# Performance work log

Measured on AMD Instinct MI355X. Metric: run time of the kernel, lower is better.

Reference implementation:

```python
import jax, jax.numpy as jnp
import numpy as np

TEMP = 0.05
EPS_SOFTMAX = 1e-6
EPS_LOG = 1e-6


def setup_inputs() -> dict:
    key = jax.random.key(0)
    k1, k2, k3, k4, k5 = jax.random.split(key, 5)
    B, F, N, C = 256, 128, 200000, 1000
    inputs = jax.random.normal(k1, (B, F), dtype=jnp.float32)
    inputs_s = jax.random.normal(k2, (B, F), dtype=jnp.float32)
    features = jax.random.normal(k3, (N, F), dtype=jnp.float32)
    # memory banks are kept L2-normalized (see MB.backward renorm)
    features = features / jnp.linalg.norm(features, axis=1, keepdims=True)
    labels = jax.random.randint(k4, (N,), 0, C, dtype=jnp.int64)
    indexes = jax.random.randint(k5, (B,), 0, N, dtype=jnp.int64)
    return {"inputs": inputs, "inputs_s": inputs_s, "features": features,
            "labels": labels, "indexes": indexes, "k": 10, "num_classes": C}


def reference(inputs, inputs_s, features, labels, indexes, k, num_classes):
    B = inputs.shape[0]
    N = features.shape[0]
    # features is a buffer (no grad in torch); MB backward also treats it as constant
    feats = jax.lax.stop_gradient(features)

    # MB.forward: inputs @ features.T, then /temp  -> [B, N]
    inputs_out = (inputs @ feats.T) / TEMP

    # local similarity [B, B]
    local = inputs @ inputs_s.T
    # topk neighbors in the bank, gather + per-sample bmm, sum over k -> [B, 1]
    _, nb_idx = jax.lax.top_k(inputs_out, k)          # [B, k]
    nb_ftr = feats[nb_idx]                             # [B, k, F]
    _local = jnp.einsum('bf,bkf->b', inputs, nb_ftr)[:, None]  # [B, 1]
    # (local + _local) masked to diagonal, then /temp
    local = (local + _local) * jnp.eye(B, dtype=local.dtype)
    local = local / TEMP

    targets = labels[indexes]                          # [B]

    # label-bucketed segment reductions -> sim [C, B]
    sim = jax.ops.segment_sum(inputs_out.T, labels, num_segments=num_classes)
    sim = sim + jax.ops.segment_sum(local, targets, num_segments=num_classes)

    nums = jax.ops.segment_sum(jnp.ones((N, 1), jnp.float32), labels,
                               num_segments=num_classes)        # [C, 1]
    nums_help = jax.ops.segment_sum(jnp.ones((B, 1), jnp.float32), targets,
                                    num_segments=num_classes)   # [C, 1]
    nums = nums + (nums_help > 0).astype(jnp.float32) * (k + 1)

    mask = (nums > 0).astype(jnp.float32)              # [C, 1]
    sim = sim / (mask * nums + (1.0 - mask))           # broadcast over B

    # masked softmax over classes, per sample: vec [B, C], mask [1, C]
    vec = sim.T
    m = mask.T                                          # [1, C]
    exps = jnp.exp(vec) * m
    masked_sim = exps / (jnp.sum(exps, axis=1, keepdims=True) + EPS_SOFTMAX)

    logp = jnp.log(masked_sim + EPS_LOG)
    loss = -jnp.mean(logp[jnp.arange(B), targets])
    return loss
```

## Files before the change

### kernel.cpp

```cpp
#include <hip/hip_runtime.h>

#define CMAX 1024
#define BQ 256
#define FQ 128
#define TN 64
#define QCAP 512
#define NBLK_DEF 768

typedef __attribute__((ext_vector_type(8))) short bf16x8;
typedef __attribute__((ext_vector_type(4))) float f32x4;

__device__ __forceinline__ unsigned short f2bf(float f){
  unsigned u = __float_as_uint(f);
  unsigned r = (u + 0x7FFFu + ((u >> 16) & 1u)) >> 16;
  return (unsigned short)r;
}
__device__ __forceinline__ unsigned encf(float f){
  unsigned u = __float_as_uint(f);
  return (u & 0x80000000u) ? ~u : (u | 0x80000000u);
}
__device__ __forceinline__ void ins16(float (&d)[16], float v){
  #pragma unroll
  for (int j = 15; j > 0; --j) d[j] = fminf(d[j-1], fmaxf(v, d[j]));
  d[0] = fmaxf(v, d[0]);
}

__global__ void k_prep(const float* __restrict__ inputs, const float* __restrict__ inputs_s,
                       const int* __restrict__ labels, const int* __restrict__ indexes,
                       unsigned short* __restrict__ inputs_bf,
                       int* __restrict__ cnt, int* __restrict__ numsh,
                       int* __restrict__ targets, float* __restrict__ diag,
                       float* __restrict__ thr, int N)
{
  __shared__ int h[CMAX];
  int t = threadIdx.x;
  for (int c = t; c < CMAX; c += 256) h[c] = 0;
  __syncthreads();
  int idx = blockIdx.x*256 + t;
  int stride = gridDim.x*256;
  for (int n = idx; n < N; n += stride) atomicAdd(&h[labels[n]], 1);
  for (int i = idx; i < BQ*FQ; i += stride) inputs_bf[i] = f2bf(inputs[i]);
  __syncthreads();
  for (int c = t; c < CMAX; c += 256){
    int v = h[c];
    if (v) atomicAdd(&cnt[c], v);
  }
  if (blockIdx.x == 0 && t < BQ){
    int tg = labels[indexes[t]];
    targets[t] = tg;
    atomicAdd(&numsh[tg], 1);
    float s = 0.f, s2 = 0.f;
    const float4* a = (const float4*)(inputs + t*FQ);
    const float4* b = (const float4*)(inputs_s + t*FQ);
    #pragma unroll
    for (int f = 0; f < FQ/4; ++f){
      float4 x = a[f], y = b[f];
      s  += x.x*y.x + x.y*y.y + x.z*y.z + x.w*y.w;
      s2 += x.x*x.x + x.y*x.y + x.z*x.z + x.w*x.w;
    }
    diag[t] = s;
    thr[t] = 3.05f * sqrtf(s2 * (1.0f/128.0f));
  }
}

__global__ void k_scan(const int* __restrict__ cnt, int* __restrict__ cur,
                       int* __restrict__ pstart, const int* __restrict__ cptr)
{
  __shared__ int s[CMAX];
  int C = cptr[0]; if (C > CMAX) C = CMAX;
  int t = threadIdx.x;
  s[t] = (t < C) ? cnt[t] : 0;
  __syncthreads();
  for (int off = 1; off < CMAX; off <<= 1){
    int v = s[t] + ((t >= off) ? s[t - off] : 0);
    __syncthreads();
    s[t] = v;
    __syncthreads();
  }
  if (t < C){
    int e = s[t] - cnt[t];
    cur[t] = e;
    pstart[t] = e;
  }
  if (t == C-1) pstart[C] = s[t];
}

__global__ void k_scatter(const int* __restrict__ labels, int* __restrict__ cur,
                          int* __restrict__ sorted_idx, int* __restrict__ sorted_cls, int N)
{
  int idx = blockIdx.x*blockDim.x + threadIdx.x;
  int stride = gridDim.x*blockDim.x;
  for (int n = idx; n < N; n += stride){
    int c = labels[n];
    int pos = atomicAdd(&cur[c], 1);
    sorted_idx[pos] = n;
    sorted_cls[pos] = c;
  }
}

__global__ __launch_bounds__(256, 3) void k_main(
    const float* __restrict__ feats,
    const int* __restrict__ sorted_idx,
    const int* __restrict__ sorted_cls,
    const unsigned short* __restrict__ inputs_bf,
    const float* __restrict__ thr,
    const int* __restrict__ pstart,
    float* __restrict__ sim,
    float* __restrict__ topk_ws,
    const int* __restrict__ cptr,
    int N, int nblk)
{
  __shared__ unsigned short fl[TN*FQ];
  __shared__ int idx_s[TN];
  __shared__ int cls_s[TN + 1];
  __shared__ unsigned q_lds[4][QCAP];
  __shared__ int qn_lds[4];

  const int t = threadIdx.x;
  const int lane = t & 63;
  const int w = t >> 6;
  const int c16 = lane & 15;
  const int g = lane >> 4;
  const int g4 = g * 4;
  const int b0 = w * 64;
  const int rbase = t >> 5;
  const int f4 = t & 31;

  if (lane == 0) qn_lds[w] = 0;

  int C = cptr[0]; if (C > CMAX) C = CMAX;
  const int j = blockIdx.x;
  const int Tj  = (int)(((long long)j * N) / nblk);
  const int Tj1 = (int)(((long long)(j+1) * N) / nblk);
  int lo = 0, hi = C;
  while (lo < hi){ int mid = (lo+hi)>>1; if (pstart[mid] < Tj) lo = mid+1; else hi = mid; }
  const int c_lo = lo;
  hi = C;
  while (lo < hi){ int mid = (lo+hi)>>1; if (pstart[mid] < Tj1) lo = mid+1; else hi = mid; }
  const int c_hi = lo;
  const int e_lo = pstart[c_lo];
  const int e_hi = pstart[c_hi];

  if (e_lo < e_hi){
    float thrs[4];
    #pragma unroll
    for (int bt = 0; bt < 4; ++bt) thrs[bt] = thr[b0 + bt*16 + c16];
    float racc[4] = {0.f, 0.f, 0.f, 0.f};

    const int nch = (e_hi - e_lo + TN - 1) / TN;

    if (t < TN + 1){
      int pos = e_lo + t;
      if (t < TN) idx_s[t] = (pos < e_hi) ? sorted_idx[pos] : 0;
      cls_s[t] = (pos < e_hi) ? sorted_cls[pos] : -2;
    }
    __syncthreads();

    for (int m = 0; m < nch; ++m){
      const int base = e_lo + m*TN;
      const int valid = min(TN, e_hi - base);

      int ireg = 0, creg = -2;
      if (t < TN + 1){
        int pos = base + TN + t;
        if (pos < e_hi){
          if (t < TN) ireg = sorted_idx[pos];
          creg = sorted_cls[pos];
        }
      }
      const int myc  = cls_s[lane];
      const int mync = cls_s[lane + 1];
      const unsigned long long bmask = __ballot((lane < valid) && (myc != mync));

      {
        const int h0 = (f4*4) ^ (rbase << 3);
        #pragma unroll
        for (int jj = 0; jj < 8; ++jj){
          const int r = jj*8 + rbase;
          float4 v;
          if (r < valid){
            const int gi = idx_s[r];
            v = *(const float4*)(feats + (size_t)gi*FQ + f4*4);
          } else { v.x = 0.f; v.y = 0.f; v.z = 0.f; v.w = 0.f; }
          ushort4 u;
          u.x = f2bf(v.x); u.y = f2bf(v.y); u.z = f2bf(v.z); u.w = f2bf(v.w);
          *(ushort4*)&fl[r*FQ + h0] = u;
        }
      }
      __syncthreads();

      if (m + 1 < nch && t < TN + 1){
        if (t < TN) idx_s[t] = ireg;
        cls_s[t] = creg;
      }

      f32x4 acc[4][4];
      #pragma unroll
      for (int nt = 0; nt < 4; ++nt)
        #pragma unroll
        for (int bt = 0; bt < 4; ++bt)
          acc[nt][bt] = (f32x4){0.f, 0.f, 0.f, 0.f};
      #pragma unroll
      for (int ks = 0; ks < 4; ++ks){
        bf16x8 af[4], bfr[4];
        #pragma unroll
        for (int nt = 0; nt < 4; ++nt){
          int r = nt*16 + c16;
          int h2 = r*FQ + ((ks*32 + g*8) ^ ((r & 7) << 3));
          af[nt] = *(const bf16x8*)&fl[h2];
        }
        #pragma unroll
        for (int bt = 0; bt < 4; ++bt){
          int b = b0 + bt*16 + c16;
          bfr[bt] = *(const bf16x8*)&inputs_bf[b*FQ + ks*32 + g*8];
        }
        #pragma unroll
        for (int nt = 0; nt < 4; ++nt)
          #pragma unroll
          for (int bt = 0; bt < 4; ++bt)
            acc[nt][bt] = __builtin_amdgcn_mfma_f32_16x16x32_bf16(af[nt], bfr[bt], acc[nt][bt], 0, 0, 0);
      }

      #pragma unroll
      for (int bt = 0; bt < 4; ++bt){
        float smax = -INFINITY;
        #pragma unroll
        for (int nt = 0; nt < 4; ++nt)
          #pragma unroll
          for (int r = 0; r < 4; ++r)
            smax = fmaxf(smax, acc[nt][bt][r]);
        if (smax > thrs[bt]){
          #pragma unroll
          for (int nt = 0; nt < 4; ++nt)
            #pragma unroll
            for (int r = 0; r < 4; ++r){
              float v = acc[nt][bt][r];
              if (v > thrs[bt]){
                int pos = atomicAdd(&qn_lds[w], 1);
                if (pos < QCAP)
                  q_lds[w][pos] = (__float_as_uint(v) & 0xFFFFFF00u) | (unsigned)(bt*16 + c16);
              }
            }
        }
      }

      if (bmask == 0ull){
        #pragma unroll
        for (int bt = 0; bt < 4; ++bt){
          float ss = 0.f;
          #pragma unroll
          for (int nt = 0; nt < 4; ++nt)
            #pragma unroll
            for (int r = 0; r < 4; ++r)
              ss += acc[nt][bt][r];
          ss += __shfl_xor(ss, 16, 64);
          ss += __shfl_xor(ss, 32, 64);
          racc[bt] += ss;
        }
      } else {
        int seglo = 0;
        unsigned long long mm = bmask;
        while (mm){
          const int p = (int)__builtin_ctzll(mm);
          float s4[4];
          #pragma unroll
          for (int bt = 0; bt < 4; ++bt){
            float ss = 0.f;
            #pragma unroll
            for (int nt = 0; nt < 4; ++nt)
              #pragma unroll
              for (int r = 0; r < 4; ++r){
                int n = nt*16 + g4 + r;
                ss += ((n >= seglo) && (n <= p)) ? acc[nt][bt][r] : 0.f;
              }
            ss += __shfl_xor(ss, 16, 64);
            ss += __shfl_xor(ss, 32, 64);
            if (seglo == 0) ss += racc[bt];
            s4[bt] = ss;
          }
          const int c = __shfl(myc, p, 64);
          if (g == 0){
            #pragma unroll
            for (int bt = 0; bt < 4; ++bt)
              sim[(size_t)c*BQ + b0 + bt*16 + c16] = s4[bt];
          }
          seglo = p + 1;
          mm &= mm - 1;
        }
        #pragma unroll
        for (int bt = 0; bt < 4; ++bt){
          float ss = 0.f;
          #pragma unroll
          for (int nt = 0; nt < 4; ++nt)
            #pragma unroll
            for (int r = 0; r < 4; ++r){
              int n = nt*16 + g4 + r;
              ss += (n >= seglo) ? acc[nt][bt][r] : 0.f;
            }
          ss += __shfl_xor(ss, 16, 64);
          ss += __shfl_xor(ss, 32, 64);
          racc[bt] = ss;
        }
      }

      __syncthreads();
    }
  }

  __builtin_amdgcn_wave_barrier();
  asm volatile("s_waitcnt lgkmcnt(0)" ::: "memory");
  __builtin_amdgcn_sched_barrier(0);
  float d[16];
  #pragma unroll
  for (int i2 = 0; i2 < 16; ++i2) d[i2] = -INFINITY;
  int qn = qn_lds[w];
  if (qn > QCAP) qn = QCAP;
  for (int qi = 0; qi < qn; ++qi){
    unsigned pk = q_lds[w][qi];
    if ((int)(pk & 0xFFu) == lane){
      float v = __uint_as_float(pk & 0xFFFFFF00u);
      if (v > d[15]) ins16(d, v);
    }
  }
  #pragma unroll
  for (int i2 = 0; i2 < 16; ++i2)
    topk_ws[((size_t)blockIdx.x*BQ + t)*16 + i2] = d[i2];
}

__global__ void k_merge(const float* __restrict__ topk_ws, int NB,
                        const float* __restrict__ diag, const int* __restrict__ targets,
                        float* __restrict__ sim, const int* __restrict__ kptr)
{
  __shared__ float Ld[4][64][16];
  const int t = threadIdx.x;
  const int lane = t & 63;
  const int w = t >> 6;
  const int b = blockIdx.x*4 + w;

  float d[16];
  #pragma unroll
  for (int j = 0; j < 16; ++j) d[j] = -INFINITY;
  for (int bk = lane; bk < NB; bk += 64){
    const float* src = topk_ws + ((size_t)bk*BQ + b)*16;
    for (int j = 0; j < 16; ++j){
      float v = src[j];
      if (!(v > d[15])) break;
      ins16(d, v);
    }
  }
  #pragma unroll
  for (int j = 0; j < 16; ++j) Ld[w][lane][j] = d[j];
  __syncthreads();
  int kk = kptr[0]; if (kk > 16) kk = 16;
  int h = 0;
  float myhead = Ld[w][lane][0];
  float tops = 0.f;
  for (int p = 0; p < 16; ++p){
    unsigned pk = (encf(myhead) & 0xFFFFFFC0u) | (unsigned)lane;
    #pragma unroll
    for (int s = 32; s > 0; s >>= 1){
      unsigned o = (unsigned)__shfl_xor((int)pk, s, 64);
      pk = (o > pk) ? o : pk;
    }
    int wl = (int)(pk & 63u);
    float val = __shfl(myhead, wl, 64);
    if (p < kk) tops += val;
    if (lane == wl){
      ++h;
      myhead = (h < 16) ? Ld[w][lane][h] : -INFINITY;
    }
  }
  if (lane == 0){
    atomicAdd(&sim[(size_t)targets[b]*BQ + b], diag[b] + tops);
  }
}

__global__ void k_expsum(const float* __restrict__ sim, const int* __restrict__ cnt,
                         const int* __restrict__ numsh, const int* __restrict__ targets,
                         const int* __restrict__ kptr, const int* __restrict__ cptr,
                         float* __restrict__ esum, float* __restrict__ etgt)
{
  int t = threadIdx.x;
  int C = cptr[0]; if (C > CMAX) C = CMAX;
  int kk = kptr[0];
  int tgt = targets[t];
  float local = 0.f;
  const float invT = 20.0f;
  for (int c = blockIdx.x; c < C; c += gridDim.x){
    float nums = (float)cnt[c] + ((numsh[c] > 0) ? (float)(kk + 1) : 0.f);
    float denom = (nums > 0.f) ? nums : 1.f;
    float val = sim[(size_t)c*BQ + t] * invT / denom;
    float e = (nums > 0.f) ? expf(val) : 0.f;
    local += e;
    if (c == tgt) etgt[t] = e;
  }
  atomicAdd(&esum[t], local);
}

__global__ void k_loss(const float* __restrict__ esum, const float* __restrict__ etgt,
                       float* __restrict__ out)
{
  __shared__ float red[BQ];
  int t = threadIdx.x;
  float p = etgt[t] / (esum[t] + 1e-6f);
  float l = -logf(p + 1e-6f);
  red[t] = l;
  __syncthreads();
  for (int off = 128; off > 0; off >>= 1){
    if (t < off) red[t] += red[t + off];
    __syncthreads();
  }
  if (t == 0) out[0] = red[0] / 256.0f;
}

extern "C" void kernel_launch(void* const* d_in, const int* in_sizes, int n_in,
                              void* d_out, int out_size, void* d_ws, size_t ws_size,
                              hipStream_t stream) {
  const float* inputs   = (const float*)d_in[0];
  const float* inputs_s = (const float*)d_in[1];
  const float* feats    = (const float*)d_in[2];
  const int*   labels   = (const int*)d_in[3];
  const int*   indexes  = (const int*)d_in[4];
  const int*   kptr     = (const int*)d_in[5];
  const int*   cptr     = (const int*)d_in[6];
  const int N = in_sizes[3];

  char* ws = (char*)d_ws;
  int*      cnt       = (int*)(ws + 0);
  int*      numsh     = (int*)(ws + 4096);
  float*    esum      = (float*)(ws + 8192);
  float*    etgt      = (float*)(ws + 9216);
  int*      targets   = (int*)(ws + 10240);
  float*    diag      = (float*)(ws + 11264);
  float*    thr       = (float*)(ws + 12288);
  int*      cur       = (int*)(ws + 13312);
  int*      pstart    = (int*)(ws + 17408);
  unsigned short* inputs_bf = (unsigned short*)(ws + 21760);
  float*    sim       = (float*)(ws + 87296);
  int*      sorted_idx = (int*)(ws + 1135872);
  int*      sorted_cls = sorted_idx + N;
  size_t off_topk = (1135872 + 8*(size_t)N + 255) & ~(size_t)255;
  float*    topk      = (float*)(ws + off_topk);

  int nblk = NBLK_DEF;
  long long topk_cap = ((long long)ws_size - (long long)off_topk) / (BQ*16*4);
  if (topk_cap < nblk) nblk = (int)topk_cap;
  if (nblk < 1) nblk = 1;
  int gN = (N + 255) / 256; if (gN > 128) gN = 128; if (gN < 1) gN = 1;

  hipMemsetAsync(ws, 0, 10240, stream);
  k_prep<<<64, 256, 0, stream>>>(inputs, inputs_s, labels, indexes, inputs_bf,
                                 cnt, numsh, targets, diag, thr, N);
  k_scan<<<1, 1024, 0, stream>>>(cnt, cur, pstart, cptr);
  k_scatter<<<gN, 256, 0, stream>>>(labels, cur, sorted_idx, sorted_cls, N);
  k_main<<<nblk, 256, 0, stream>>>(feats, sorted_idx, sorted_cls, inputs_bf, thr,
                                   pstart, sim, topk, cptr, N, nblk);
  k_merge<<<BQ/4, 256, 0, stream>>>(topk, nblk, diag, targets, sim, kptr);
  k_expsum<<<64, 256, 0, stream>>>(sim, cnt, numsh, targets, kptr, cptr, esum, etgt);
  k_loss<<<1, 256, 0, stream>>>(esum, etgt, (float*)d_out);
}
```

Measured before the change: 204.8 us.

## Replace class-aligned partitioning with fixed chunks, sliced atomic sim, global candidate top-k

The main GEMM kernel no longer partitions work by class boundaries with binary search. Each block now walks fixed 64-row chunks and atomically adds per-class segment sums into one of 8 replicated sim slices, which k_expsum sums back together. The per-block 16-deep top-k arrays and the merge kernel are replaced by a global candidate list of above-threshold scores, and a per-sample k_topk kernel scans that list. This is meant to balance load and cut top-k workspace traffic. In exchange it adds zeroing of 8MB of slices, float atomics, a full scan of the candidate list for each of the 256 samples, and a truncation risk at QCAP or CCAP.

```diff
diff --git a/kernel.cpp b/kernel.cpp
--- a/kernel.cpp
+++ b/kernel.cpp
@@ -4,8 +4,9 @@
 #define BQ 256
 #define FQ 128
 #define TN 64
-#define QCAP 512
-#define NBLK_DEF 768
+#define QCAP 256
+#define NSLICE 8
+#define CCAP 131072
 
 typedef __attribute__((ext_vector_type(8))) short bf16x8;
 typedef __attribute__((ext_vector_type(4))) float f32x4;
@@ -15,19 +16,10 @@
   unsigned r = (u + 0x7FFFu + ((u >> 16) & 1u)) >> 16;
   return (unsigned short)r;
 }
-__device__ __forceinline__ unsigned encf(float f){
-  unsigned u = __float_as_uint(f);
-  return (u & 0x80000000u) ? ~u : (u | 0x80000000u);
-}
-__device__ __forceinline__ void ins16(float (&d)[16], float v){
-  #pragma unroll
-  for (int j = 15; j > 0; --j) d[j] = fminf(d[j-1], fmaxf(v, d[j]));
-  d[0] = fmaxf(v, d[0]);
-}
 
 __global__ void k_prep(const float* __restrict__ inputs, const float* __restrict__ inputs_s,
                        const int* __restrict__ labels, const int* __restrict__ indexes,
-                       unsigned short* __restrict__ inputs_bf,
+                       unsigned short* __restrict__ inputs_bf, float4* __restrict__ sim8_4,
                        int* __restrict__ cnt, int* __restrict__ numsh,
                        int* __restrict__ targets, float* __restrict__ diag,
                        float* __restrict__ thr, int N)
@@ -38,6 +30,8 @@
   __syncthreads();
   int idx = blockIdx.x*256 + t;
   int stride = gridDim.x*256;
+  float4 z; z.x = z.y = z.z = z.w = 0.f;
+  for (int i = idx; i < NSLICE*CMAX*BQ/4; i += stride) sim8_4[i] = z;
   for (int n = idx; n < N; n += stride) atomicAdd(&h[labels[n]], 1);
   for (int i = idx; i < BQ*FQ; i += stride) inputs_bf[i] = f2bf(inputs[i]);
   __syncthreads();
@@ -64,7 +58,7 @@
 }
 
 __global__ void k_scan(const int* __restrict__ cnt, int* __restrict__ cur,
-                       int* __restrict__ pstart, const int* __restrict__ cptr)
+                       const int* __restrict__ cptr)
 {
   __shared__ int s[CMAX];
   int C = cptr[0]; if (C > CMAX) C = CMAX;
@@ -77,12 +71,7 @@
     s[t] = v;
     __syncthreads();
   }
-  if (t < C){
-    int e = s[t] - cnt[t];
-    cur[t] = e;
-    pstart[t] = e;
-  }
-  if (t == C-1) pstart[C] = s[t];
+  if (t < C) cur[t] = s[t] - cnt[t];
 }
 
 __global__ void k_scatter(const int* __restrict__ labels, int* __restrict__ cur,
@@ -104,15 +93,14 @@
     const int* __restrict__ sorted_cls,
     const unsigned short* __restrict__ inputs_bf,
     const float* __restrict__ thr,
-    const int* __restrict__ pstart,
-    float* __restrict__ sim,
-    float* __restrict__ topk_ws,
-    const int* __restrict__ cptr,
-    int N, int nblk)
+    float* __restrict__ sim8,
+    unsigned* __restrict__ cands,
+    int* __restrict__ gcount,
+    int N, int NCHUNK, int nblk)
 {
   __shared__ unsigned short fl[TN*FQ];
   __shared__ int idx_s[TN];
-  __shared__ int cls_s[TN + 1];
+  __shared__ int cls_s[TN];
   __shared__ unsigned q_lds[4][QCAP];
   __shared__ int qn_lds[4];
 
@@ -127,166 +115,101 @@
   const int f4 = t & 31;
 
   if (lane == 0) qn_lds[w] = 0;
-
-  int C = cptr[0]; if (C > CMAX) C = CMAX;
-  const int j = blockIdx.x;
-  const int Tj  = (int)(((long long)j * N) / nblk);
-  const int Tj1 = (int)(((long long)(j+1) * N) / nblk);
-  int lo = 0, hi = C;
-  while (lo < hi){ int mid = (lo+hi)>>1; if (pstart[mid] < Tj) lo = mid+1; else hi = mid; }
-  const int c_lo = lo;
-  hi = C;
-  while (lo < hi){ int mid = (lo+hi)>>1; if (pstart[mid] < Tj1) lo = mid+1; else hi = mid; }
-  const int c_hi = lo;
-  const int e_lo = pstart[c_lo];
-  const int e_hi = pstart[c_hi];
-
-  if (e_lo < e_hi){
-    float thrs[4];
-    #pragma unroll
-    for (int bt = 0; bt < 4; ++bt) thrs[bt] = thr[b0 + bt*16 + c16];
-    float racc[4] = {0.f, 0.f, 0.f, 0.f};
-
-    const int nch = (e_hi - e_lo + TN - 1) / TN;
-
-    if (t < TN + 1){
-      int pos = e_lo + t;
-      if (t < TN) idx_s[t] = (pos < e_hi) ? sorted_idx[pos] : 0;
-      cls_s[t] = (pos < e_hi) ? sorted_cls[pos] : -2;
-    }
-    __syncthreads();
-
-    for (int m = 0; m < nch; ++m){
-      const int base = e_lo + m*TN;
-      const int valid = min(TN, e_hi - base);
-
-      int ireg = 0, creg = -2;
-      if (t < TN + 1){
-        int pos = base + TN + t;
-        if (pos < e_hi){
-          if (t < TN) ireg = sorted_idx[pos];
-          creg = sorted_cls[pos];
-        }
-      }
-      const int myc  = cls_s[lane];
-      const int mync = cls_s[lane + 1];
-      const unsigned long long bmask = __ballot((lane < valid) && (myc != mync));
-
-      {
-        const int h0 = (f4*4) ^ (rbase << 3);
-        #pragma unroll
-        for (int jj = 0; jj < 8; ++jj){
-          const int r = jj*8 + rbase;
-          float4 v;
-          if (r < valid){
-            const int gi = idx_s[r];
-            v = *(const float4*)(feats + (size_t)gi*FQ + f4*4);
-          } else { v.x = 0.f; v.y = 0.f; v.z = 0.f; v.w = 0.f; }
-          ushort4 u;
-          u.x = f2bf(v.x); u.y = f2bf(v.y); u.z = f2bf(v.z); u.w = f2bf(v.w);
-          *(ushort4*)&fl[r*FQ + h0] = u;
-        }
-      }
-      __syncthreads();
-
-      if (m + 1 < nch && t < TN + 1){
-        if (t < TN) idx_s[t] = ireg;
-        cls_s[t] = creg;
-      }
-
-      f32x4 acc[4][4];
+  float* sim_sl = sim8 + (size_t)(blockIdx.x & (NSLICE-1)) * CMAX * BQ;
+
+  float thrs[4];
+  #pragma unroll
+  for (int bt = 0; bt < 4; ++bt) thrs[bt] = thr[b0 + bt*16 + c16];
+
+  for (int chunk = blockIdx.x; chunk < NCHUNK; chunk += nblk){
+    const int base = chunk * TN;
+    const int valid = min(TN, N - base);
+
+    if (t < TN){
+      int pos = base + t;
+      bool live = (pos < N);
+      idx_s[t] = live ? sorted_idx[pos] : 0;
+      cls_s[t] = live ? sorted_cls[pos] : -1;
+    }
+    __syncthreads();
+
+    {
+      const int h0 = (f4*4) ^ (rbase << 3);
+      #pragma unroll
+      for (int jj = 0; jj < 8; ++jj){
+        const int r = jj*8 + rbase;
+        float4 v;
+        if (r < valid){
+          const int gi = idx_s[r];
+          v = *(const float4*)(feats + (size_t)gi*FQ + f4*4);
+        } else { v.x = 0.f; v.y = 0.f; v.z = 0.f; v.w = 0.f; }
+        ushort4 u;
+        u.x = f2bf(v.x); u.y = f2bf(v.y); u.z = f2bf(v.z); u.w = f2bf(v.w);
+        *(ushort4*)&fl[r*FQ + h0] = u;
+      }
+    }
+    const int myc  = (lane < valid) ? cls_s[lane] : -1;
+    const bool bnd = (lane < valid) &&
+                     ((lane == valid-1) || (cls_s[lane+1] != myc));
+    const unsigned long long bmask = __ballot(bnd);
+    __syncthreads();
+
+    f32x4 acc[4][4];
+    #pragma unroll
+    for (int nt = 0; nt < 4; ++nt)
+      #pragma unroll
+      for (int bt = 0; bt < 4; ++bt)
+        acc[nt][bt] = (f32x4){0.f, 0.f, 0.f, 0.f};
+    #pragma unroll
+    for (int ks = 0; ks < 4; ++ks){
+      bf16x8 af[4], bfr[4];
+      #pragma unroll
+      for (int nt = 0; nt < 4; ++nt){
+        int r = nt*16 + c16;
+        int h2 = r*FQ + ((ks*32 + g*8) ^ ((r & 7) << 3));
+        af[nt] = *(const bf16x8*)&fl[h2];
+      }
+      #pragma unroll
+      for (int bt = 0; bt < 4; ++bt){
+        int b = b0 + bt*16 + c16;
+        bfr[bt] = *(const bf16x8*)&inputs_bf[b*FQ + ks*32 + g*8];
+      }
       #pragma unroll
       for (int nt = 0; nt < 4; ++nt)
         #pragma unroll
         for (int bt = 0; bt < 4; ++bt)
-          acc[nt][bt] = (f32x4){0.f, 0.f, 0.f, 0.f};
-      #pragma unroll
-      for (int ks = 0; ks < 4; ++ks){
-        bf16x8 af[4], bfr[4];
+          acc[nt][bt] = __builtin_amdgcn_mfma_f32_16x16x32_bf16(af[nt], bfr[bt], acc[nt][bt], 0, 0, 0);
+    }
+
+    #pragma unroll
+    for (int bt = 0; bt < 4; ++bt){
+      float smax = -INFINITY;
+      #pragma unroll
+      for (int nt = 0; nt < 4; ++nt)
         #pragma unroll
-        for (int nt = 0; nt < 4; ++nt){
-          int r = nt*16 + c16;
-          int h2 = r*FQ + ((ks*32 + g*8) ^ ((r & 7) << 3));
-          af[nt] = *(const bf16x8*)&fl[h2];
-        }
-        #pragma unroll
-        for (int bt = 0; bt < 4; ++bt){
-          int b = b0 + bt*16 + c16;
-          bfr[bt] = *(const bf16x8*)&inputs_bf[b*FQ + ks*32 + g*8];
-        }
+        for (int r = 0; r < 4; ++r)
+          smax = fmaxf(smax, acc[nt][bt][r]);
+      if (smax > thrs[bt]){
         #pragma unroll
         for (int nt = 0; nt < 4; ++nt)
           #pragma unroll
-          for (int bt = 0; bt < 4; ++bt)
-            acc[nt][bt] = __builtin_amdgcn_mfma_f32_16x16x32_bf16(af[nt], bfr[bt], acc[nt][bt], 0, 0, 0);
-      }
-
-      #pragma unroll
-      for (int bt = 0; bt < 4; ++bt){
-        float smax = -INFINITY;
-        #pragma unroll
-        for (int nt = 0; nt < 4; ++nt)
-          #pragma unroll
-          for (int r = 0; r < 4; ++r)
-            smax = fmaxf(smax, acc[nt][bt][r]);
-        if (smax > thrs[bt]){
-          #pragma unroll
-          for (int nt = 0; nt < 4; ++nt)
-            #pragma unroll
-            for (int r = 0; r < 4; ++r){
-              float v = acc[nt][bt][r];
-              if (v > thrs[bt]){
-                int pos = atomicAdd(&qn_lds[w], 1);
-                if (pos < QCAP)
-                  q_lds[w][pos] = (__float_as_uint(v) & 0xFFFFFF00u) | (unsigned)(bt*16 + c16);
-              }
+          for (int r = 0; r < 4; ++r){
+            float v = acc[nt][bt][r];
+            if (v > thrs[bt]){
+              int pos = atomicAdd(&qn_lds[w], 1);
+              if (pos < QCAP)
+                q_lds[w][pos] = (__float_as_uint(v) & 0xFFFFFF00u) | (unsigned)(b0 + bt*16 + c16);
             }
-        }
-      }
-
-      if (bmask == 0ull){
-        #pragma unroll
-        for (int bt = 0; bt < 4; ++bt){
-          float ss = 0.f;
-          #pragma unroll
-          for (int nt = 0; nt < 4; ++nt)
-            #pragma unroll
-            for (int r = 0; r < 4; ++r)
-              ss += acc[nt][bt][r];
-          ss += __shfl_xor(ss, 16, 64);
-          ss += __shfl_xor(ss, 32, 64);
-          racc[bt] += ss;
-        }
-      } else {
-        int seglo = 0;
-        unsigned long long mm = bmask;
-        while (mm){
-          const int p = (int)__builtin_ctzll(mm);
-          float s4[4];
-          #pragma unroll
-          for (int bt = 0; bt < 4; ++bt){
-            float ss = 0.f;
-            #pragma unroll
-            for (int nt = 0; nt < 4; ++nt)
-              #pragma unroll
-              for (int r = 0; r < 4; ++r){
-                int n = nt*16 + g4 + r;
-                ss += ((n >= seglo) && (n <= p)) ? acc[nt][bt][r] : 0.f;
-              }
-            ss += __shfl_xor(ss, 16, 64);
-            ss += __shfl_xor(ss, 32, 64);
-            if (seglo == 0) ss += racc[bt];
-            s4[bt] = ss;
           }
-          const int c = __shfl(myc, p, 64);
-          if (g == 0){
-            #pragma unroll
-            for (int bt = 0; bt < 4; ++bt)
-              sim[(size_t)c*BQ + b0 + bt*16 + c16] = s4[bt];
-          }
-          seglo = p + 1;
-          mm &= mm - 1;
-        }
+      }
+    }
+
+    {
+      int seglo = 0;
+      unsigned long long mm = bmask;
+      while (mm){
+        const int p = (int)__builtin_ctzll(mm);
+        float s4[4];
         #pragma unroll
         for (int bt = 0; bt < 4; ++bt){
           float ss = 0.f;
@@ -295,87 +218,88 @@
             #pragma unroll
             for (int r = 0; r < 4; ++r){
               int n = nt*16 + g4 + r;
-              ss += (n >= seglo) ? acc[nt][bt][r] : 0.f;
+              ss += ((n >= seglo) && (n <= p)) ? acc[nt][bt][r] : 0.f;
             }
           ss += __shfl_xor(ss, 16, 64);
           ss += __shfl_xor(ss, 32, 64);
-          racc[bt] = ss;
+          s4[bt] = ss;
         }
-      }
-
-      __syncthreads();
-    }
+        const int c = __shfl(myc, p, 64);
+        if (g == 0){
+          #pragma unroll
+          for (int bt = 0; bt < 4; ++bt)
+            atomicAdd(&sim_sl[(size_t)c*BQ + b0 + bt*16 + c16], s4[bt]);
+        }
+        seglo = p + 1;
+        mm &= mm - 1;
+      }
+    }
+    __syncthreads();
   }
 
   __builtin_amdgcn_wave_barrier();
   asm volatile("s_waitcnt lgkmcnt(0)" ::: "memory");
-  __builtin_amdgcn_sched_barrier(0);
-  float d[16];
-  #pragma unroll
-  for (int i2 = 0; i2 < 16; ++i2) d[i2] = -INFINITY;
   int qn = qn_lds[w];
   if (qn > QCAP) qn = QCAP;
-  for (int qi = 0; qi < qn; ++qi){
-    unsigned pk = q_lds[w][qi];
-    if ((int)(pk & 0xFFu) == lane){
-      float v = __uint_as_float(pk & 0xFFFFFF00u);
-      if (v > d[15]) ins16(d, v);
-    }
-  }
-  #pragma unroll
-  for (int i2 = 0; i2 < 16; ++i2)
-    topk_ws[((size_t)blockIdx.x*BQ + t)*16 + i2] = d[i2];
-}
-
-__global__ void k_merge(const float* __restrict__ topk_ws, int NB,
-                        const float* __restrict__ diag, const int* __restrict__ targets,
-                        float* __restrict__ sim, const int* __restrict__ kptr)
-{
-  __shared__ float Ld[4][64][16];
+  int base_g = 0;
+  if (qn > 0){
+    if (lane == 0) base_g = atomicAdd(gcount, qn);
+    base_g = __shfl(base_g, 0, 64);
+    for (int i = lane; i < qn; i += 64){
+      int p = base_g + i;
+      if (p < CCAP) cands[p] = q_lds[w][i];
+    }
+  }
+}
+
+__global__ void k_topk(const unsigned* __restrict__ cands, const int* __restrict__ gcount,
+                       const float* __restrict__ diag, const int* __restrict__ targets,
+                       float* __restrict__ sim8, const int* __restrict__ kptr)
+{
+  __shared__ unsigned lst[2048];
+  __shared__ int cnt_s;
   const int t = threadIdx.x;
-  const int lane = t & 63;
-  const int w = t >> 6;
-  const int b = blockIdx.x*4 + w;
-
-  float d[16];
-  #pragma unroll
-  for (int j = 0; j < 16; ++j) d[j] = -INFINITY;
-  for (int bk = lane; bk < NB; bk += 64){
-    const float* src = topk_ws + ((size_t)bk*BQ + b)*16;
-    for (int j = 0; j < 16; ++j){
-      float v = src[j];
-      if (!(v > d[15])) break;
-      ins16(d, v);
-    }
-  }
-  #pragma unroll
-  for (int j = 0; j < 16; ++j) Ld[w][lane][j] = d[j];
-  __syncthreads();
-  int kk = kptr[0]; if (kk > 16) kk = 16;
-  int h = 0;
-  float myhead = Ld[w][lane][0];
-  float tops = 0.f;
-  for (int p = 0; p < 16; ++p){
-    unsigned pk = (encf(myhead) & 0xFFFFFFC0u) | (unsigned)lane;
-    #pragma unroll
-    for (int s = 32; s > 0; s >>= 1){
-      unsigned o = (unsigned)__shfl_xor((int)pk, s, 64);
-      pk = (o > pk) ? o : pk;
-    }
-    int wl = (int)(pk & 63u);
-    float val = __shfl(myhead, wl, 64);
-    if (p < kk) tops += val;
-    if (lane == wl){
-      ++h;
-      myhead = (h < 16) ? Ld[w][lane][h] : -INFINITY;
-    }
-  }
-  if (lane == 0){
-    atomicAdd(&sim[(size_t)targets[b]*BQ + b], diag[b] + tops);
-  }
-}
-
-__global__ void k_expsum(const float* __restrict__ sim, const int* __restrict__ cnt,
+  const int b = blockIdx.x;
+  if (t == 0) cnt_s = 0;
+  __syncthreads();
+  int total = gcount[0]; if (total > CCAP) total = CCAP;
+  for (int i = t; i < total; i += 256){
+    unsigned pk = cands[i];
+    if ((int)(pk & 0xFFu) == b){
+      int p = atomicAdd(&cnt_s, 1);
+      if (p < 2048) lst[p] = pk;
+    }
+  }
+  __syncthreads();
+  if (t < 64){
+    int n = cnt_s; if (n > 2048) n = 2048;
+    int kk = kptr[0]; if (kk > 16) kk = 16;
+    float tops = 0.f;
+    for (int p = 0; p < kk; ++p){
+      unsigned best = 0; int bi = -1;
+      for (int i = t; i < n; i += 64){
+        unsigned v = lst[i];
+        if (v > best){ best = v; bi = i; }
+      }
+      unsigned key = (best & 0xFFFFFF00u) | (unsigned)t;
+      #pragma unroll
+      for (int s = 32; s > 0; s >>= 1){
+        unsigned o = (unsigned)__shfl_xor((int)key, s, 64);
+        key = (o > key) ? o : key;
+      }
+      int wl = (int)(key & 63u);
+      int bidx = __shfl(bi, wl, 64);
+      tops += __uint_as_float(key & 0xFFFFFF00u);
+      if (t == wl && bidx >= 0) lst[bidx] = 0;
+      __builtin_amdgcn_wave_barrier();
+      asm volatile("s_waitcnt lgkmcnt(0)" ::: "memory");
+    }
+    if (t == 0)
+      atomicAdd(&sim8[(size_t)targets[b]*BQ + b], diag[b] + tops);
+  }
+}
+
+__global__ void k_expsum(const float* __restrict__ sim8, const int* __restrict__ cnt,
                          const int* __restrict__ numsh, const int* __restrict__ targets,
                          const int* __restrict__ kptr, const int* __restrict__ cptr,
                          float* __restrict__ esum, float* __restrict__ etgt)
@@ -387,9 +311,13 @@
   float local = 0.f;
   const float invT = 20.0f;
   for (int c = blockIdx.x; c < C; c += gridDim.x){
+    float v = 0.f;
+    #pragma unroll
+    for (int p = 0; p < NSLICE; ++p)
+      v += sim8[(size_t)p*CMAX*BQ + (size_t)c*BQ + t];
     float nums = (float)cnt[c] + ((numsh[c] > 0) ? (float)(kk + 1) : 0.f);
     float denom = (nums > 0.f) ? nums : 1.f;
-    float val = sim[(size_t)c*BQ + t] * invT / denom;
+    float val = v * invT / denom;
     float e = (nums > 0.f) ? expf(val) : 0.f;
     local += e;
     if (c == tgt) etgt[t] = e;
@@ -430,32 +358,31 @@
   int*      numsh     = (int*)(ws + 4096);
   float*    esum      = (float*)(ws + 8192);
   float*    etgt      = (float*)(ws + 9216);
-  int*      targets   = (int*)(ws + 10240);
-  float*    diag      = (float*)(ws + 11264);
-  float*    thr       = (float*)(ws + 12288);
-  int*      cur       = (int*)(ws + 13312);
-  int*      pstart    = (int*)(ws + 17408);
-  unsigned short* inputs_bf = (unsigned short*)(ws + 21760);
-  float*    sim       = (float*)(ws + 87296);
-  int*      sorted_idx = (int*)(ws + 1135872);
+  int*      gcount    = (int*)(ws + 10240);
+  int*      targets   = (int*)(ws + 10496);
+  float*    diag      = (float*)(ws + 11520);
+  float*    thr       = (float*)(ws + 12544);
+  int*      cur       = (int*)(ws + 13568);
+  unsigned short* inputs_bf = (unsigned short*)(ws + 17664);
+  float*    sim8      = (float*)(ws + 83200);
+  int*      sorted_idx = (int*)(ws + 83200 + (size_t)NSLICE*CMAX*BQ*4);
   int*      sorted_cls = sorted_idx + N;
-  size_t off_topk = (1135872 + 8*(size_t)N + 255) & ~(size_t)255;
-  float*    topk      = (float*)(ws + off_topk);
-
-  int nblk = NBLK_DEF;
-  long long topk_cap = ((long long)ws_size - (long long)off_topk) / (BQ*16*4);
-  if (topk_cap < nblk) nblk = (int)topk_cap;
+  unsigned* cands     = (unsigned*)((char*)(sorted_cls + N));
+
+  const int NCHUNK = (N + TN - 1) / TN;
+  int nblk = (NCHUNK + 1) / 2;
   if (nblk < 1) nblk = 1;
+  if (nblk > 4096) nblk = 4096;
   int gN = (N + 255) / 256; if (gN > 128) gN = 128; if (gN < 1) gN = 1;
 
-  hipMemsetAsync(ws, 0, 10240, stream);
+  hipMemsetAsync(ws, 0, 10496, stream);
   k_prep<<<64, 256, 0, stream>>>(inputs, inputs_s, labels, indexes, inputs_bf,
-                                 cnt, numsh, targets, diag, thr, N);
-  k_scan<<<1, 1024, 0, stream>>>(cnt, cur, pstart, cptr);
+                                 (float4*)sim8, cnt, numsh, targets, diag, thr, N);
+  k_scan<<<1, 1024, 0, stream>>>(cnt, cur, cptr);
   k_scatter<<<gN, 256, 0, stream>>>(labels, cur, sorted_idx, sorted_cls, N);
   k_main<<<nblk, 256, 0, stream>>>(feats, sorted_idx, sorted_cls, inputs_bf, thr,
-                                   pstart, sim, topk, cptr, N, nblk);
-  k_merge<<<BQ/4, 256, 0, stream>>>(topk, nblk, diag, targets, sim, kptr);
-  k_expsum<<<64, 256, 0, stream>>>(sim, cnt, numsh, targets, kptr, cptr, esum, etgt);
+                                   sim8, cands, gcount, N, NCHUNK, nblk);
+  k_topk<<<BQ, 256, 0, stream>>>(cands, gcount, diag, targets, sim8, kptr);
+  k_expsum<<<64, 256, 0, stream>>>(sim8, cnt, numsh, targets, kptr, cptr, esum, etgt);
   k_loss<<<1, 256, 0, stream>>>(esum, etgt, (float*)d_out);
 }
```

Result: slower. 325.6 us (+59.0%).
